# Performance work log

Measured on AMD Instinct MI355X. Metric: run time of the kernel, lower is better.

## Reference

```python
import jax, jax.numpy as jnp
import numpy as np

B, C, D = 2, 2048, 1024   # batch, seq_len, hidden_size
I = 2048                  # intermediate_size (GLU hidden)
E, K = 8, 2               # n_experts, top_k
CF = 1.25                 # capacity factor


def setup_inputs() -> dict:
    key = jax.random.key(0)
    k1, k2, k3, k4 = jax.random.split(key, 4)
    scale = 0.02
    return {
        "hidden_states": jax.random.normal(k1, (B, C, D), jnp.float32),
        "Wg": jax.random.normal(k2, (E, D), jnp.float32) * scale,      # router gate weight [E, d]
        "W1": jax.random.normal(k3, (E, D, 2 * I), jnp.float32) * scale,  # expert in-proj
        "W2": jax.random.normal(k4, (E, I, D), jnp.float32) * scale,      # expert out-proj
    }


def reference(hidden_states, Wg, W1, W2):
    Bx, Cx, d = hidden_states.shape
    N = Bx * Cx
    cap = int(N * K * CF / E)  # exp_capacity (static)
    x = hidden_states.reshape(N, d)

    # --- router (eval mode: no noise) ---
    logits = x @ Wg.T                          # [N, E]
    top_v, top_i = jax.lax.top_k(logits, K)    # [N, K]
    gates = jax.nn.softmax(top_v, axis=-1)     # [N, K]

    # --- greedy capacity-limited assignment (token-major, then k), vectorized ---
    flat_e = top_i.reshape(N * K)              # expert id per (token, k) slot, in loop order
    gates_f = gates.reshape(N * K)
    tok = jnp.repeat(jnp.arange(N), K)         # token id per slot
    onehot = jax.nn.one_hot(flat_e, E, dtype=jnp.int32)
    pos = jnp.cumsum(onehot, axis=0) - 1       # running count per expert
    pos_f = jnp.take_along_axis(pos, flat_e[:, None], axis=1)[:, 0]
    keep = pos_f < cap                         # slots beyond capacity are dropped
    pos_safe = jnp.where(keep, pos_f, cap)     # out-of-range -> dropped by mode='drop'

    # --- dispatch: exp_batches[e, pos] = x[token] ---
    exp_batches = jnp.zeros((E, cap, d), x.dtype).at[flat_e, pos_safe].set(x[tok], mode='drop')

    # --- per-expert GLU MLP (batched over experts) ---
    h = jnp.einsum('ecd,edf->ecf', exp_batches, W1)       # [E, cap, 2I]
    inp, gate = jnp.split(h, 2, axis=-1)
    h = jax.nn.gelu(inp, approximate=False) * gate        # exact gelu, matches torch
    exp_out = jnp.einsum('eci,eid->ecd', h, W2)           # [E, cap, d]

    # --- combine: equals exp_mask.view(N,-1) @ exp_out.view(-1,d) ---
    gathered = exp_out[flat_e, jnp.minimum(pos_safe, cap - 1)]  # [N*K, d]
    contrib = jnp.where(keep, gates_f, 0.0)[:, None] * gathered
    out = jax.ops.segment_sum(contrib, tok, num_segments=N)    # [N, d]
    return out.reshape(Bx, Cx, d)
```

## Files before the change

kernel.cpp:

```cpp
#include <hip/hip_runtime.h>
#include <hip/hip_bf16.h>
#include <math.h>

#define N_TOK 4096
#define DIM   1024
#define NEXP  8
#define IDIM  2048
#define TWOI  4096
#define CAP   1280

#define W1_BLOCKS (64 * 16 * NEXP)
#define W2_BLOCKS (16 * 32 * NEXP)

using short8  = __attribute__((ext_vector_type(8))) short;
using floatx4 = __attribute__((ext_vector_type(4))) float;

__device__ __forceinline__ unsigned short f2b(float f) {
  __hip_bfloat16 h = __float2bfloat16(f);
  return *reinterpret_cast<unsigned short*>(&h);
}

__device__ __forceinline__ void async16(const unsigned short* g, unsigned short* l) {
  __builtin_amdgcn_global_load_lds(
      (const __attribute__((address_space(1))) unsigned int*)g,
      (__attribute__((address_space(3))) unsigned int*)l,
      16, 0, 0);
}

__global__ __launch_bounds__(256) void trans_kernel(const float* __restrict__ W1,
                                                    const float* __restrict__ W2,
                                                    unsigned short* __restrict__ w1t,
                                                    unsigned short* __restrict__ w2t) {
  __shared__ float tile[64][65];
  int bid = blockIdx.x;
  const float* s; unsigned short* d; int R, C, r0, c0;
  if (bid < W1_BLOCKS) {
    int e = bid >> 10;
    int t = bid & 1023;
    R = DIM; C = TWOI;
    r0 = (t & 15) * 64;
    c0 = (t >> 4) * 64;
    s = W1 + (size_t)e * R * C;
    d = w1t + (size_t)e * R * C;
  } else {
    int b2 = bid - W1_BLOCKS;
    int e = b2 >> 9;
    int t = b2 & 511;
    R = IDIM; C = DIM;
    r0 = (t & 31) * 64;
    c0 = (t >> 5) * 64;
    s = W2 + (size_t)e * R * C;
    d = w2t + (size_t)e * R * C;
  }
  int tid = threadIdx.x;
  int tr = tid >> 4, tc = (tid & 15) * 4;
#pragma unroll
  for (int i = 0; i < 4; i++) {
    float4 v = *reinterpret_cast<const float4*>(&s[(size_t)(r0 + tr + i * 16) * C + c0 + tc]);
    tile[tr + i * 16][tc]     = v.x;
    tile[tr + i * 16][tc + 1] = v.y;
    tile[tr + i * 16][tc + 2] = v.z;
    tile[tr + i * 16][tc + 3] = v.w;
  }
  __syncthreads();
#pragma unroll
  for (int j = 0; j < 4; j++) {
    int c = (tid >> 4) + j * 16;
    int r4 = (tid & 15) * 4;
    ushort4 o;
    o.x = f2b(tile[r4][c]);
    o.y = f2b(tile[r4 + 1][c]);
    o.z = f2b(tile[r4 + 2][c]);
    o.w = f2b(tile[r4 + 3][c]);
    *reinterpret_cast<ushort4*>(&d[(size_t)(c0 + c) * R + r0 + r4]) = o;
  }
}

__global__ __launch_bounds__(256) void router_kernel(const float* __restrict__ x,
                                                     const float* __restrict__ Wg,
                                                     unsigned short* __restrict__ xb,
                                                     float* __restrict__ out,
                                                     int* __restrict__ top_i,
                                                     float* __restrict__ gates) {
  __shared__ float wg[NEXP * DIM];
  int tid = threadIdx.x;
  for (int i = tid * 4; i < NEXP * DIM; i += 256 * 4) {
    *reinterpret_cast<float4*>(wg + i) = *reinterpret_cast<const float4*>(Wg + i);
  }
  __syncthreads();
  int wave = tid >> 6, lane = tid & 63;
  int t = blockIdx.x * 4 + wave;
  const float* xr = x + (size_t)t * DIM;
  unsigned short* xbr = xb + (size_t)t * DIM;
  float* outr = out + (size_t)t * DIM;
  double acc[NEXP];
#pragma unroll
  for (int e = 0; e < NEXP; e++) acc[e] = 0.0;
  for (int i = lane; i < DIM; i += 64) {
    float xf = xr[i];
    xbr[i] = f2b(xf);
    outr[i] = 0.0f;
    double xv = (double)xf;
#pragma unroll
    for (int e = 0; e < NEXP; e++) acc[e] += xv * (double)wg[e * DIM + i];
  }
#pragma unroll
  for (int e = 0; e < NEXP; e++) {
#pragma unroll
    for (int m = 1; m < 64; m <<= 1) acc[e] += __shfl_xor(acc[e], m, 64);
  }
  if (lane == 0) {
    int i0 = 0; double v0 = acc[0];
    for (int e = 1; e < NEXP; e++) { if (acc[e] > v0) { v0 = acc[e]; i0 = e; } }
    int i1 = -1; double v1 = -1e300;
    for (int e = 0; e < NEXP; e++) { if (e != i0 && acc[e] > v1) { v1 = acc[e]; i1 = e; } }
    double e1 = exp(v1 - v0);
    float g0 = (float)(1.0 / (1.0 + e1));
    float g1 = (float)(e1 / (1.0 + e1));
    top_i[t * 2] = i0; top_i[t * 2 + 1] = i1;
    gates[t * 2] = g0; gates[t * 2 + 1] = g1;
  }
}

__global__ __launch_bounds__(1024) void scan_kernel(const int* __restrict__ top_i,
                                                    const float* __restrict__ gates,
                                                    int* __restrict__ rowtok,
                                                    float* __restrict__ rowgate,
                                                    int* __restrict__ cnt) {
  __shared__ int hist[NEXP][1024];
  int t = threadIdx.x;
  int s0 = t * 8;
  int eloc[8];
  int c[NEXP];
#pragma unroll
  for (int e = 0; e < NEXP; e++) c[e] = 0;
#pragma unroll
  for (int j = 0; j < 8; j++) { int e = top_i[s0 + j]; eloc[j] = e; c[e]++; }
#pragma unroll
  for (int e = 0; e < NEXP; e++) hist[e][t] = c[e];
  __syncthreads();
  for (int step = 1; step < 1024; step <<= 1) {
    int tmp[NEXP];
#pragma unroll
    for (int e = 0; e < NEXP; e++) tmp[e] = (t >= step) ? hist[e][t - step] : 0;
    __syncthreads();
#pragma unroll
    for (int e = 0; e < NEXP; e++) hist[e][t] += tmp[e];
    __syncthreads();
  }
  int base[NEXP];
#pragma unroll
  for (int e = 0; e < NEXP; e++) base[e] = hist[e][t] - c[e];
  if (t < NEXP) {
    int tot = hist[t][1023];
    cnt[t] = tot < CAP ? tot : CAP;
  }
#pragma unroll
  for (int j = 0; j < 8; j++) {
    int s = s0 + j;
    int e = eloc[j];
    int pos = base[e]++;
    if (pos < CAP) {
      rowtok[e * CAP + pos] = s >> 1;
      rowgate[e * CAP + pos] = gates[s];
    }
  }
}

__global__ __launch_bounds__(256, 3) void gemm1_kernel(const unsigned short* __restrict__ xb,
                                                       const unsigned short* __restrict__ w1t,
                                                       const int* __restrict__ rowtok,
                                                       const int* __restrict__ cnt,
                                                       unsigned short* __restrict__ H) {
  int e  = blockIdx.z;
  int m0 = blockIdx.y * 128;
  int i0 = blockIdx.x * 64;
  int cnte = cnt[e];
  if (m0 >= cnte) return;

  __shared__ __align__(16) unsigned short As[128 * 32];
  __shared__ __align__(16) unsigned short Bi[64 * 32];
  __shared__ __align__(16) unsigned short Bg[64 * 32];

  int tid  = threadIdx.x;
  int lane = tid & 63;
  int wave = tid >> 6;

  int srA0 = wave * 32 + (lane >> 2);
  int srA1 = srA0 + 16;
  int srB  = wave * 16 + (lane >> 2);
  int sk   = (lane & 3) * 8;

  int ma0 = m0 + srA0, ma1 = m0 + srA1;
  int tok0 = (ma0 < cnte) ? rowtok[e * CAP + ma0] : 0;
  int tok1 = (ma1 < cnte) ? rowtok[e * CAP + ma1] : 0;

  const unsigned short* w1e = w1t + (size_t)e * TWOI * DIM;
  const unsigned short* gA0 = xb + (size_t)tok0 * DIM + sk;
  const unsigned short* gA1 = xb + (size_t)tok1 * DIM + sk;
  const unsigned short* gBi = w1e + (size_t)(i0 + srB) * DIM + sk;
  const unsigned short* gBg = w1e + (size_t)(i0 + srB + IDIM) * DIM + sk;

  unsigned short* lA0 = As + (wave * 2 + 0) * 512;
  unsigned short* lA1 = As + (wave * 2 + 1) * 512;
  unsigned short* lBi = Bi + wave * 512;
  unsigned short* lBg = Bg + wave * 512;

  int lane16 = lane & 15;
  int quad   = lane >> 4;
  int wm = (wave & 1) * 64;
  int wn = (wave >> 1) * 32;

  floatx4 acc_i[4][2], acc_g[4][2];
#pragma unroll
  for (int i = 0; i < 4; i++)
#pragma unroll
    for (int j = 0; j < 2; j++) {
      acc_i[i][j] = (floatx4){0.f, 0.f, 0.f, 0.f};
      acc_g[i][j] = (floatx4){0.f, 0.f, 0.f, 0.f};
    }

  for (int k0 = 0; k0 < DIM; k0 += 32) {
    __syncthreads();
    async16(gA0 + k0, lA0);
    async16(gA1 + k0, lA1);
    async16(gBi + k0, lBi);
    async16(gBg + k0, lBg);
    __syncthreads();

    short8 a[4];
#pragma unroll
    for (int i = 0; i < 4; i++)
      a[i] = *(const short8*)&As[(wm + i * 16 + lane16) * 32 + quad * 8];
#pragma unroll
    for (int j = 0; j < 2; j++) {
      short8 bi = *(const short8*)&Bi[(wn + j * 16 + lane16) * 32 + quad * 8];
#pragma unroll
      for (int i = 0; i < 4; i++)
        acc_i[i][j] = __builtin_amdgcn_mfma_f32_16x16x32_bf16(a[i], bi, acc_i[i][j], 0, 0, 0);
      short8 bg = *(const short8*)&Bg[(wn + j * 16 + lane16) * 32 + quad * 8];
#pragma unroll
      for (int i = 0; i < 4; i++)
        acc_g[i][j] = __builtin_amdgcn_mfma_f32_16x16x32_bf16(a[i], bg, acc_g[i][j], 0, 0, 0);
    }
  }

  unsigned short* He = H + (size_t)e * CAP * IDIM;
#pragma unroll
  for (int i = 0; i < 4; i++) {
#pragma unroll
    for (int r = 0; r < 4; r++) {
      int m = m0 + wm + i * 16 + quad * 4 + r;
#pragma unroll
      for (int j = 0; j < 2; j++) {
        int n = i0 + wn + j * 16 + lane16;
        float vi = acc_i[i][j][r];
        float vg = acc_g[i][j][r];
        float h = 0.5f * vi * (1.0f + erff(vi * 0.70710678118654752f)) * vg;
        He[(size_t)m * IDIM + n] = f2b(h);
      }
    }
  }
}

__global__ __launch_bounds__(256, 3) void gemm2_kernel(const unsigned short* __restrict__ H,
                                                       const unsigned short* __restrict__ w2t,
                                                       const int* __restrict__ cnt,
                                                       const int* __restrict__ rowtok,
                                                       const float* __restrict__ rowgate,
                                                       float* __restrict__ out) {
  int e  = blockIdx.z;
  int m0 = blockIdx.y * 128;
  int n0 = blockIdx.x * 128;
  int cnte = cnt[e];
  if (m0 >= cnte) return;

  __shared__ __align__(16) unsigned short As[128 * 32];
  __shared__ __align__(16) unsigned short Bs[128 * 32];

  int tid  = threadIdx.x;
  int lane = tid & 63;
  int wave = tid >> 6;

  int sr0 = wave * 32 + (lane >> 2);
  int sr1 = sr0 + 16;
  int sk  = (lane & 3) * 8;

  const unsigned short* He  = H + (size_t)e * CAP * IDIM;
  const unsigned short* w2e = w2t + (size_t)e * DIM * IDIM;
  const unsigned short* gA0 = He + (size_t)(m0 + sr0) * IDIM + sk;
  const unsigned short* gA1 = He + (size_t)(m0 + sr1) * IDIM + sk;
  const unsigned short* gB0 = w2e + (size_t)(n0 + sr0) * IDIM + sk;
  const unsigned short* gB1 = w2e + (size_t)(n0 + sr1) * IDIM + sk;

  unsigned short* lA0 = As + (wave * 2 + 0) * 512;
  unsigned short* lA1 = As + (wave * 2 + 1) * 512;
  unsigned short* lB0 = Bs + (wave * 2 + 0) * 512;
  unsigned short* lB1 = Bs + (wave * 2 + 1) * 512;

  int lane16 = lane & 15;
  int quad   = lane >> 4;
  int wm = (wave & 1) * 64;
  int wn = (wave >> 1) * 64;

  floatx4 acc[4][4];
#pragma unroll
  for (int i = 0; i < 4; i++)
#pragma unroll
    for (int j = 0; j < 4; j++) acc[i][j] = (floatx4){0.f, 0.f, 0.f, 0.f};

  for (int k0 = 0; k0 < IDIM; k0 += 32) {
    __syncthreads();
    async16(gA0 + k0, lA0);
    async16(gA1 + k0, lA1);
    async16(gB0 + k0, lB0);
    async16(gB1 + k0, lB1);
    __syncthreads();

    short8 a[4];
#pragma unroll
    for (int i = 0; i < 4; i++)
      a[i] = *(const short8*)&As[(wm + i * 16 + lane16) * 32 + quad * 8];
#pragma unroll
    for (int j = 0; j < 4; j++) {
      short8 b = *(const short8*)&Bs[(wn + j * 16 + lane16) * 32 + quad * 8];
#pragma unroll
      for (int i = 0; i < 4; i++)
        acc[i][j] = __builtin_amdgcn_mfma_f32_16x16x32_bf16(a[i], b, acc[i][j], 0, 0, 0);
    }
  }

#pragma unroll
  for (int i = 0; i < 4; i++) {
#pragma unroll
    for (int r = 0; r < 4; r++) {
      int m = m0 + wm + i * 16 + quad * 4 + r;
      if (m < cnte) {
        int tok = rowtok[e * CAP + m];
        float g = rowgate[e * CAP + m];
        float* orow = out + (size_t)tok * DIM;
#pragma unroll
        for (int j = 0; j < 4; j++) {
          int n = n0 + wn + j * 16 + lane16;
          atomicAdd(orow + n, g * acc[i][j][r]);
        }
      }
    }
  }
}

extern "C" void kernel_launch(void* const* d_in, const int* in_sizes, int n_in,
                              void* d_out, int out_size, void* d_ws, size_t ws_size,
                              hipStream_t stream) {
  const float* x  = (const float*)d_in[0];
  const float* Wg = (const float*)d_in[1];
  const float* W1 = (const float*)d_in[2];
  const float* W2 = (const float*)d_in[3];
  float* out = (float*)d_out;

  char* ws = (char*)d_ws;
  size_t off = 0;
  auto alloc = [&](size_t bytes) -> void* {
    void* p = ws + off;
    off = (off + bytes + 255) & ~(size_t)255;
    return p;
  };
  int*   top_i   = (int*)alloc((size_t)N_TOK * 2 * sizeof(int));
  float* gates   = (float*)alloc((size_t)N_TOK * 2 * sizeof(float));
  int*   rowtok  = (int*)alloc((size_t)NEXP * CAP * sizeof(int));
  float* rowgate = (float*)alloc((size_t)NEXP * CAP * sizeof(float));
  int*   cnt     = (int*)alloc((size_t)NEXP * sizeof(int));
  unsigned short* xb  = (unsigned short*)alloc((size_t)N_TOK * DIM * 2);
  unsigned short* w1t = (unsigned short*)alloc((size_t)NEXP * TWOI * DIM * 2);
  unsigned short* w2t = (unsigned short*)alloc((size_t)NEXP * DIM * IDIM * 2);
  unsigned short* Hb  = (unsigned short*)alloc((size_t)NEXP * CAP * IDIM * 2);
  if (off > ws_size) return;

  hipLaunchKernelGGL(trans_kernel, dim3(W1_BLOCKS + W2_BLOCKS), dim3(256), 0, stream,
                     W1, W2, w1t, w2t);
  hipLaunchKernelGGL(router_kernel, dim3(N_TOK / 4), dim3(256), 0, stream,
                     x, Wg, xb, out, top_i, gates);
  hipLaunchKernelGGL(scan_kernel, dim3(1), dim3(1024), 0, stream,
                     top_i, gates, rowtok, rowgate, cnt);
  hipLaunchKernelGGL(gemm1_kernel, dim3(IDIM / 64, CAP / 128, NEXP), dim3(256), 0, stream,
                     xb, w1t, rowtok, cnt, Hb);
  hipLaunchKernelGGL(gemm2_kernel, dim3(DIM / 128, CAP / 128, NEXP), dim3(256), 0, stream,
                     Hb, w2t, cnt, rowtok, rowgate, out);
}
```

Baseline: 468.8 us.

## Fuse transpose and router into one prologue kernel, shrink gemm2 N-tile

Merges the weight transpose/convert kernel and the router kernel into a single launch that picks its role by block index, so router work overlaps with transposition and one launch is removed. The shared block is now sized for the router (32KB), which may lower occupancy for the transpose blocks. gemm2 moves from 128x128 to 128x64 tiles to double the grid, and both GEMMs raise their launch-bounds occupancy hint from 3 to 4 blocks, which may force register spills in gemm1.

```diff
diff --git a/kernel.cpp b/kernel.cpp
--- a/kernel.cpp
+++ b/kernel.cpp
@@ -11,6 +11,8 @@
 
 #define W1_BLOCKS (64 * 16 * NEXP)
 #define W2_BLOCKS (16 * 32 * NEXP)
+#define TRANS_TOTAL (W1_BLOCKS + W2_BLOCKS)
+#define ROUTER_BLOCKS (N_TOK / 4)
 
 using short8  = __attribute__((ext_vector_type(8))) short;
 using floatx4 = __attribute__((ext_vector_type(4))) float;
@@ -27,98 +29,101 @@
       16, 0, 0);
 }
 
-__global__ __launch_bounds__(256) void trans_kernel(const float* __restrict__ W1,
-                                                    const float* __restrict__ W2,
-                                                    unsigned short* __restrict__ w1t,
-                                                    unsigned short* __restrict__ w2t) {
-  __shared__ float tile[64][65];
+__global__ __launch_bounds__(256) void prologue_kernel(const float* __restrict__ W1,
+                                                       const float* __restrict__ W2,
+                                                       unsigned short* __restrict__ w1t,
+                                                       unsigned short* __restrict__ w2t,
+                                                       const float* __restrict__ x,
+                                                       const float* __restrict__ Wg,
+                                                       unsigned short* __restrict__ xb,
+                                                       float* __restrict__ out,
+                                                       int* __restrict__ top_i,
+                                                       float* __restrict__ gates) {
+  __shared__ __align__(16) float smem_f[NEXP * DIM];
   int bid = blockIdx.x;
-  const float* s; unsigned short* d; int R, C, r0, c0;
-  if (bid < W1_BLOCKS) {
-    int e = bid >> 10;
-    int t = bid & 1023;
-    R = DIM; C = TWOI;
-    r0 = (t & 15) * 64;
-    c0 = (t >> 4) * 64;
-    s = W1 + (size_t)e * R * C;
-    d = w1t + (size_t)e * R * C;
+  int tid = threadIdx.x;
+
+  if (bid < TRANS_TOTAL) {
+    float (*tile)[65] = reinterpret_cast<float (*)[65]>(smem_f);
+    const float* s; unsigned short* d; int R, C, r0, c0;
+    if (bid < W1_BLOCKS) {
+      int e = bid >> 10;
+      int t = bid & 1023;
+      R = DIM; C = TWOI;
+      r0 = (t & 15) * 64;
+      c0 = (t >> 4) * 64;
+      s = W1 + (size_t)e * R * C;
+      d = w1t + (size_t)e * R * C;
+    } else {
+      int b2 = bid - W1_BLOCKS;
+      int e = b2 >> 9;
+      int t = b2 & 511;
+      R = IDIM; C = DIM;
+      r0 = (t & 31) * 64;
+      c0 = (t >> 5) * 64;
+      s = W2 + (size_t)e * R * C;
+      d = w2t + (size_t)e * R * C;
+    }
+    int tr = tid >> 4, tc = (tid & 15) * 4;
+#pragma unroll
+    for (int i = 0; i < 4; i++) {
+      float4 v = *reinterpret_cast<const float4*>(&s[(size_t)(r0 + tr + i * 16) * C + c0 + tc]);
+      tile[tr + i * 16][tc]     = v.x;
+      tile[tr + i * 16][tc + 1] = v.y;
+      tile[tr + i * 16][tc + 2] = v.z;
+      tile[tr + i * 16][tc + 3] = v.w;
+    }
+    __syncthreads();
+#pragma unroll
+    for (int j = 0; j < 4; j++) {
+      int c = (tid >> 4) + j * 16;
+      int r4 = (tid & 15) * 4;
+      ushort4 o;
+      o.x = f2b(tile[r4][c]);
+      o.y = f2b(tile[r4 + 1][c]);
+      o.z = f2b(tile[r4 + 2][c]);
+      o.w = f2b(tile[r4 + 3][c]);
+      *reinterpret_cast<ushort4*>(&d[(size_t)(c0 + c) * R + r0 + r4]) = o;
+    }
   } else {
-    int b2 = bid - W1_BLOCKS;
-    int e = b2 >> 9;
-    int t = b2 & 511;
-    R = IDIM; C = DIM;
-    r0 = (t & 31) * 64;
-    c0 = (t >> 5) * 64;
-    s = W2 + (size_t)e * R * C;
-    d = w2t + (size_t)e * R * C;
-  }
-  int tid = threadIdx.x;
-  int tr = tid >> 4, tc = (tid & 15) * 4;
-#pragma unroll
-  for (int i = 0; i < 4; i++) {
-    float4 v = *reinterpret_cast<const float4*>(&s[(size_t)(r0 + tr + i * 16) * C + c0 + tc]);
-    tile[tr + i * 16][tc]     = v.x;
-    tile[tr + i * 16][tc + 1] = v.y;
-    tile[tr + i * 16][tc + 2] = v.z;
-    tile[tr + i * 16][tc + 3] = v.w;
-  }
-  __syncthreads();
-#pragma unroll
-  for (int j = 0; j < 4; j++) {
-    int c = (tid >> 4) + j * 16;
-    int r4 = (tid & 15) * 4;
-    ushort4 o;
-    o.x = f2b(tile[r4][c]);
-    o.y = f2b(tile[r4 + 1][c]);
-    o.z = f2b(tile[r4 + 2][c]);
-    o.w = f2b(tile[r4 + 3][c]);
-    *reinterpret_cast<ushort4*>(&d[(size_t)(c0 + c) * R + r0 + r4]) = o;
-  }
-}
-
-__global__ __launch_bounds__(256) void router_kernel(const float* __restrict__ x,
-                                                     const float* __restrict__ Wg,
-                                                     unsigned short* __restrict__ xb,
-                                                     float* __restrict__ out,
-                                                     int* __restrict__ top_i,
-                                                     float* __restrict__ gates) {
-  __shared__ float wg[NEXP * DIM];
-  int tid = threadIdx.x;
-  for (int i = tid * 4; i < NEXP * DIM; i += 256 * 4) {
-    *reinterpret_cast<float4*>(wg + i) = *reinterpret_cast<const float4*>(Wg + i);
-  }
-  __syncthreads();
-  int wave = tid >> 6, lane = tid & 63;
-  int t = blockIdx.x * 4 + wave;
-  const float* xr = x + (size_t)t * DIM;
-  unsigned short* xbr = xb + (size_t)t * DIM;
-  float* outr = out + (size_t)t * DIM;
-  double acc[NEXP];
-#pragma unroll
-  for (int e = 0; e < NEXP; e++) acc[e] = 0.0;
-  for (int i = lane; i < DIM; i += 64) {
-    float xf = xr[i];
-    xbr[i] = f2b(xf);
-    outr[i] = 0.0f;
-    double xv = (double)xf;
-#pragma unroll
-    for (int e = 0; e < NEXP; e++) acc[e] += xv * (double)wg[e * DIM + i];
-  }
-#pragma unroll
-  for (int e = 0; e < NEXP; e++) {
-#pragma unroll
-    for (int m = 1; m < 64; m <<= 1) acc[e] += __shfl_xor(acc[e], m, 64);
-  }
-  if (lane == 0) {
-    int i0 = 0; double v0 = acc[0];
-    for (int e = 1; e < NEXP; e++) { if (acc[e] > v0) { v0 = acc[e]; i0 = e; } }
-    int i1 = -1; double v1 = -1e300;
-    for (int e = 0; e < NEXP; e++) { if (e != i0 && acc[e] > v1) { v1 = acc[e]; i1 = e; } }
-    double e1 = exp(v1 - v0);
-    float g0 = (float)(1.0 / (1.0 + e1));
-    float g1 = (float)(e1 / (1.0 + e1));
-    top_i[t * 2] = i0; top_i[t * 2 + 1] = i1;
-    gates[t * 2] = g0; gates[t * 2 + 1] = g1;
+    int rb = bid - TRANS_TOTAL;
+    float* wg = smem_f;
+    for (int i = tid * 4; i < NEXP * DIM; i += 256 * 4) {
+      *reinterpret_cast<float4*>(wg + i) = *reinterpret_cast<const float4*>(Wg + i);
+    }
+    __syncthreads();
+    int wave = tid >> 6, lane = tid & 63;
+    int t = rb * 4 + wave;
+    const float* xr = x + (size_t)t * DIM;
+    unsigned short* xbr = xb + (size_t)t * DIM;
+    float* outr = out + (size_t)t * DIM;
+    double acc[NEXP];
+#pragma unroll
+    for (int e = 0; e < NEXP; e++) acc[e] = 0.0;
+    for (int i = lane; i < DIM; i += 64) {
+      float xf = xr[i];
+      xbr[i] = f2b(xf);
+      outr[i] = 0.0f;
+      double xv = (double)xf;
+#pragma unroll
+      for (int e = 0; e < NEXP; e++) acc[e] += xv * (double)wg[e * DIM + i];
+    }
+#pragma unroll
+    for (int e = 0; e < NEXP; e++) {
+#pragma unroll
+      for (int m = 1; m < 64; m <<= 1) acc[e] += __shfl_xor(acc[e], m, 64);
+    }
+    if (lane == 0) {
+      int i0 = 0; double v0 = acc[0];
+      for (int e = 1; e < NEXP; e++) { if (acc[e] > v0) { v0 = acc[e]; i0 = e; } }
+      int i1 = -1; double v1 = -1e300;
+      for (int e = 0; e < NEXP; e++) { if (e != i0 && acc[e] > v1) { v1 = acc[e]; i1 = e; } }
+      double e1 = exp(v1 - v0);
+      float g0 = (float)(1.0 / (1.0 + e1));
+      float g1 = (float)(e1 / (1.0 + e1));
+      top_i[t * 2] = i0; top_i[t * 2 + 1] = i1;
+      gates[t * 2] = g0; gates[t * 2 + 1] = g1;
+    }
   }
 }
 
@@ -167,7 +172,7 @@
   }
 }
 
-__global__ __launch_bounds__(256, 3) void gemm1_kernel(const unsigned short* __restrict__ xb,
+__global__ __launch_bounds__(256, 4) void gemm1_kernel(const unsigned short* __restrict__ xb,
                                                        const unsigned short* __restrict__ w1t,
                                                        const int* __restrict__ rowtok,
                                                        const int* __restrict__ cnt,
@@ -263,7 +268,7 @@
   }
 }
 
-__global__ __launch_bounds__(256, 3) void gemm2_kernel(const unsigned short* __restrict__ H,
+__global__ __launch_bounds__(256, 4) void gemm2_kernel(const unsigned short* __restrict__ H,
                                                        const unsigned short* __restrict__ w2t,
                                                        const int* __restrict__ cnt,
                                                        const int* __restrict__ rowtok,
@@ -271,12 +276,12 @@
                                                        float* __restrict__ out) {
   int e  = blockIdx.z;
   int m0 = blockIdx.y * 128;
-  int n0 = blockIdx.x * 128;
+  int n0 = blockIdx.x * 64;
   int cnte = cnt[e];
   if (m0 >= cnte) return;
 
   __shared__ __align__(16) unsigned short As[128 * 32];
-  __shared__ __align__(16) unsigned short Bs[128 * 32];
+  __shared__ __align__(16) unsigned short Bs[64 * 32];
 
   int tid  = threadIdx.x;
   int lane = tid & 63;
@@ -284,37 +289,35 @@
 
   int sr0 = wave * 32 + (lane >> 2);
   int sr1 = sr0 + 16;
+  int srB = wave * 16 + (lane >> 2);
   int sk  = (lane & 3) * 8;
 
   const unsigned short* He  = H + (size_t)e * CAP * IDIM;
   const unsigned short* w2e = w2t + (size_t)e * DIM * IDIM;
   const unsigned short* gA0 = He + (size_t)(m0 + sr0) * IDIM + sk;
   const unsigned short* gA1 = He + (size_t)(m0 + sr1) * IDIM + sk;
-  const unsigned short* gB0 = w2e + (size_t)(n0 + sr0) * IDIM + sk;
-  const unsigned short* gB1 = w2e + (size_t)(n0 + sr1) * IDIM + sk;
+  const unsigned short* gB  = w2e + (size_t)(n0 + srB) * IDIM + sk;
 
   unsigned short* lA0 = As + (wave * 2 + 0) * 512;
   unsigned short* lA1 = As + (wave * 2 + 1) * 512;
-  unsigned short* lB0 = Bs + (wave * 2 + 0) * 512;
-  unsigned short* lB1 = Bs + (wave * 2 + 1) * 512;
+  unsigned short* lB  = Bs + wave * 512;
 
   int lane16 = lane & 15;
   int quad   = lane >> 4;
   int wm = (wave & 1) * 64;
-  int wn = (wave >> 1) * 64;
-
-  floatx4 acc[4][4];
+  int wn = (wave >> 1) * 32;
+
+  floatx4 acc[4][2];
 #pragma unroll
   for (int i = 0; i < 4; i++)
 #pragma unroll
-    for (int j = 0; j < 4; j++) acc[i][j] = (floatx4){0.f, 0.f, 0.f, 0.f};
+    for (int j = 0; j < 2; j++) acc[i][j] = (floatx4){0.f, 0.f, 0.f, 0.f};
 
   for (int k0 = 0; k0 < IDIM; k0 += 32) {
     __syncthreads();
     async16(gA0 + k0, lA0);
     async16(gA1 + k0, lA1);
-    async16(gB0 + k0, lB0);
-    async16(gB1 + k0, lB1);
+    async16(gB + k0, lB);
     __syncthreads();
 
     short8 a[4];
@@ -322,7 +325,7 @@
     for (int i = 0; i < 4; i++)
       a[i] = *(const short8*)&As[(wm + i * 16 + lane16) * 32 + quad * 8];
 #pragma unroll
-    for (int j = 0; j < 4; j++) {
+    for (int j = 0; j < 2; j++) {
       short8 b = *(const short8*)&Bs[(wn + j * 16 + lane16) * 32 + quad * 8];
 #pragma unroll
       for (int i = 0; i < 4; i++)
@@ -340,7 +343,7 @@
         float g = rowgate[e * CAP + m];
         float* orow = out + (size_t)tok * DIM;
 #pragma unroll
-        for (int j = 0; j < 4; j++) {
+        for (int j = 0; j < 2; j++) {
           int n = n0 + wn + j * 16 + lane16;
           atomicAdd(orow + n, g * acc[i][j][r]);
         }
@@ -376,14 +379,12 @@
   unsigned short* Hb  = (unsigned short*)alloc((size_t)NEXP * CAP * IDIM * 2);
   if (off > ws_size) return;
 
-  hipLaunchKernelGGL(trans_kernel, dim3(W1_BLOCKS + W2_BLOCKS), dim3(256), 0, stream,
-                     W1, W2, w1t, w2t);
-  hipLaunchKernelGGL(router_kernel, dim3(N_TOK / 4), dim3(256), 0, stream,
-                     x, Wg, xb, out, top_i, gates);
+  hipLaunchKernelGGL(prologue_kernel, dim3(TRANS_TOTAL + ROUTER_BLOCKS), dim3(256), 0, stream,
+                     W1, W2, w1t, w2t, x, Wg, xb, out, top_i, gates);
   hipLaunchKernelGGL(scan_kernel, dim3(1), dim3(1024), 0, stream,
                      top_i, gates, rowtok, rowgate, cnt);
   hipLaunchKernelGGL(gemm1_kernel, dim3(IDIM / 64, CAP / 128, NEXP), dim3(256), 0, stream,
                      xb, w1t, rowtok, cnt, Hb);
-  hipLaunchKernelGGL(gemm2_kernel, dim3(DIM / 128, CAP / 128, NEXP), dim3(256), 0, stream,
+  hipLaunchKernelGGL(gemm2_kernel, dim3(DIM / 64, CAP / 128, NEXP), dim3(256), 0, stream,
                      Hb, w2t, cnt, rowtok, rowgate, out);
 }
```

Result: slower. 479.6 us (+2.3%).
